# Optimization experiments

Hardware: AMD Instinct MI355X
Metric: run time of the kernel (lower is better)

## Reference

```python
import jax, jax.numpy as jnp
import numpy as np

N = 100000
E = 1600000
IN_DIM = 128
OUT_DIM = 128
NEG_SLOPE = 0.01  # F.leaky_relu default


def setup_inputs() -> dict:
    key = jax.random.key(0)
    k1, k2, k3, k4, k5, k6 = jax.random.split(key, 6)
    feat = jax.random.normal(k1, (N, IN_DIM), dtype=jnp.float32)
    biclique_mask = jax.random.uniform(k2, (IN_DIM,), dtype=jnp.float32)
    W = jax.random.normal(k3, (OUT_DIM, IN_DIM), dtype=jnp.float32) * 0.05
    attn = jax.random.normal(k4, (OUT_DIM,), dtype=jnp.float32) * 0.1
    src = jax.random.randint(k5, (E,), 0, N, dtype=jnp.int32)
    dst = jax.random.randint(k6, (E,), 0, N, dtype=jnp.int32)
    return {"feat": feat, "biclique_mask": biclique_mask, "W": W,
            "attn": attn, "src": src, "dst": dst}


def reference(feat, biclique_mask, W, attn, src, dst):
    # h = Linear(feat * mask), no bias
    h = (feat * biclique_mask[None, :]) @ W.T            # [N, out_dim]
    # edge score depends only on src node -> compute per-node then gather
    s = jax.nn.leaky_relu(h @ attn, negative_slope=NEG_SLOPE)  # [N]
    score = s[src]                                        # [E]
    # edge softmax grouped by destination node
    seg_max = jax.ops.segment_max(score, dst, num_segments=N)  # [N]
    seg_max = jnp.where(jnp.isfinite(seg_max), seg_max, 0.0)   # empty segs
    ex = jnp.exp(score - seg_max[dst])                     # [E]
    denom = jax.ops.segment_sum(ex, dst, num_segments=N)   # [N]
    a = ex / denom[dst]                                    # [E]
    # weighted aggregation: sum_{e: dst(e)=v} h[src(e)] * a[e]
    m = h[src] * a[:, None]                                # [E, out_dim]
    h_new = jax.ops.segment_sum(m, dst, num_segments=N)    # [N, out_dim]
    return jax.nn.relu(h_new)
```

## Files before the change

### kernel.cpp

```cpp
#include <hip/hip_runtime.h>
#include <math.h>

#define NN 100000
#define EE 1600000
#define DIM 128

#define BK 256
#define NBK2 392
#define NCH 256
#define EPB 6250
#define SCN (NBK2 * NCH)
#define NSB 98

#define SRC_MASK 0x1FFFFu

typedef _Float16 half8 __attribute__((ext_vector_type(8)));
typedef float f32x4 __attribute__((ext_vector_type(4)));

__global__ __launch_bounds__(256) void k_wt(const float* __restrict__ W,
                                            const float* __restrict__ mask,
                                            _Float16* __restrict__ Bt) {
    int o = blockIdx.x * 256 + threadIdx.x;
    if (o < DIM * DIM) Bt[o] = (_Float16)(W[o] * mask[o & 127]);
}

__global__ __launch_bounds__(256) void k_gemm(const float* __restrict__ feat,
                                              const _Float16* __restrict__ Bt,
                                              const float* __restrict__ attn,
                                              _Float16* __restrict__ hh,
                                              _Float16* __restrict__ sv16) {
    const int lane = threadIdx.x & 63;
    const int wv   = threadIdx.x >> 6;
    const int l15  = lane & 15;
    const int quad = lane >> 4;
    const int row0 = blockIdx.x * 64 + wv * 16;

    f32x4 acc[8];
#pragma unroll
    for (int nt = 0; nt < 8; ++nt) acc[nt] = (f32x4){0.f, 0.f, 0.f, 0.f};

    const int arow = row0 + l15;
    const bool okA = arow < NN;
    const float* ap = feat + (size_t)(okA ? arow : 0) * DIM + quad * 8;

#pragma unroll
    for (int kc = 0; kc < 4; ++kc) {
        half8 a;
        float4 f0 = ((const float4*)(ap + kc * 32))[0];
        float4 f1 = ((const float4*)(ap + kc * 32))[1];
        if (!okA) { f0 = make_float4(0, 0, 0, 0); f1 = make_float4(0, 0, 0, 0); }
        a[0] = (_Float16)f0.x; a[1] = (_Float16)f0.y;
        a[2] = (_Float16)f0.z; a[3] = (_Float16)f0.w;
        a[4] = (_Float16)f1.x; a[5] = (_Float16)f1.y;
        a[6] = (_Float16)f1.z; a[7] = (_Float16)f1.w;
#pragma unroll
        for (int nt = 0; nt < 8; ++nt) {
            half8 b = *(const half8*)(Bt + (size_t)(nt * 16 + l15) * DIM + kc * 32 + quad * 8);
            acc[nt] = __builtin_amdgcn_mfma_f32_16x16x32_f16(a, b, acc[nt], 0, 0, 0);
        }
    }

    float avv[8];
#pragma unroll
    for (int nt = 0; nt < 8; ++nt) avv[nt] = attn[nt * 16 + l15];

#pragma unroll
    for (int r = 0; r < 4; ++r) {
        int row = row0 + quad * 4 + r;
        float p = 0.f;
#pragma unroll
        for (int nt = 0; nt < 8; ++nt) p += acc[nt][r] * avv[nt];
        p += __shfl_xor(p, 1, 64);
        p += __shfl_xor(p, 2, 64);
        p += __shfl_xor(p, 4, 64);
        p += __shfl_xor(p, 8, 64);
        if (l15 == 0 && row < NN) {
            float lr = (p > 0.f) ? p : 0.01f * p;
            sv16[row] = (_Float16)__expf(lr);
        }
    }

#pragma unroll
    for (int nt = 0; nt < 8; ++nt) {
#pragma unroll
        for (int r = 0; r < 4; ++r) {
            int row = row0 + quad * 4 + r;
            if (row < NN)
                hh[(size_t)row * DIM + nt * 16 + l15] = (_Float16)acc[nt][r];
        }
    }
}

__global__ __launch_bounds__(1024) void k_bhist(const int* __restrict__ dst,
                                                int* __restrict__ gHist) {
    __shared__ int hist[NBK2];
    const int t = threadIdx.x, b = blockIdx.x;
    for (int i = t; i < NBK2; i += 1024) hist[i] = 0;
    __syncthreads();
    const int e0 = b * EPB;
    int e1 = e0 + EPB; if (e1 > EE) e1 = EE;
    for (int e = e0 + t; e < e1; e += 1024)
        atomicAdd(&hist[dst[e] >> 8], 1);
    __syncthreads();
    for (int i = t; i < NBK2; i += 1024)
        gHist[i * NCH + b] = hist[i];
}

__global__ __launch_bounds__(256) void k_scan_a(const int* __restrict__ deg,
                                                int* __restrict__ excl,
                                                int* __restrict__ bsum) {
    __shared__ int wsum[4];
    __shared__ int woff[4];
    const int t = threadIdx.x, b = blockIdx.x;
    const int base = b * 1024 + t * 4;
    int v0 = deg[base + 0];
    int v1 = deg[base + 1];
    int v2 = deg[base + 2];
    int v3 = deg[base + 3];
    int tsum = v0 + v1 + v2 + v3;

    const int lane = t & 63, w = t >> 6;
    int incl = tsum;
#pragma unroll
    for (int d = 1; d < 64; d <<= 1) {
        int n = __shfl_up(incl, d, 64);
        if (lane >= d) incl += n;
    }
    if (lane == 63) wsum[w] = incl;
    __syncthreads();
    if (t == 0) {
        int run = 0;
#pragma unroll
        for (int i = 0; i < 4; ++i) { woff[i] = run; run += wsum[i]; }
        bsum[b] = run;
    }
    __syncthreads();
    int texcl = incl - tsum + woff[w];
    excl[base + 0] = texcl;
    excl[base + 1] = texcl + v0;
    excl[base + 2] = texcl + v0 + v1;
    excl[base + 3] = texcl + v0 + v1 + v2;
}

__global__ __launch_bounds__(128) void k_scan_b(const int* __restrict__ bsum,
                                                int* __restrict__ boff) {
    __shared__ int wtop[2];
    const int t = threadIdx.x;
    const int lane = t & 63, w = t >> 6;
    int v = (t < NSB) ? bsum[t] : 0;
    int incl = v;
#pragma unroll
    for (int d = 1; d < 64; d <<= 1) {
        int n = __shfl_up(incl, d, 64);
        if (lane >= d) incl += n;
    }
    if (lane == 63) wtop[w] = incl;
    __syncthreads();
    int add = (w == 1) ? wtop[0] : 0;
    if (t < NSB) boff[t] = incl - v + add;
}

__global__ __launch_bounds__(1024) void k_bscatter(const int* __restrict__ src,
                                                   const int* __restrict__ dst,
                                                   const int* __restrict__ gOff,
                                                   const int* __restrict__ boff,
                                                   unsigned* __restrict__ binned) {
    __shared__ int cur[NBK2];
    const int t = threadIdx.x, b = blockIdx.x;
    for (int i = t; i < NBK2; i += 1024) {
        int idx = i * NCH + b;
        cur[i] = gOff[idx] + boff[idx >> 10];
    }
    __syncthreads();
    const int e0 = b * EPB;
    int e1 = e0 + EPB; if (e1 > EE) e1 = EE;
    for (int e = e0 + t; e < e1; e += 1024) {
        int d  = dst[e];
        int si = src[e];
        int bk   = d >> 8;
        int dloc = d & (BK - 1);
        int pos = atomicAdd(&cur[bk], 1);
        binned[pos] = (unsigned)si | ((unsigned)dloc << 17);
    }
}

__global__ __launch_bounds__(1024) void k_group(const int* __restrict__ gOff,
                                                const int* __restrict__ boff,
                                                const unsigned* __restrict__ binned,
                                                const _Float16* __restrict__ sv16,
                                                unsigned* __restrict__ pack,
                                                int* __restrict__ offs) {
    __shared__ int ldeg[BK];
    __shared__ int wpart[4];
    const int bk = blockIdx.x;
    const int t  = threadIdx.x;
    const int i0 = bk * NCH;
    const int base = gOff[i0] + boff[i0 >> 10];
    int endp;
    if (bk == NBK2 - 1) endp = EE;
    else {
        int i1 = (bk + 1) * NCH;
        endp = gOff[i1] + boff[i1 >> 10];
    }

    if (t < BK) ldeg[t] = 0;
    __syncthreads();
    for (int j = base + t; j < endp; j += 1024)
        atomicAdd(&ldeg[(binned[j] >> 17) & (BK - 1)], 1);
    __syncthreads();

    int v = 0, incl = 0;
    const int lane = t & 63;
    if (t < BK) {
        v = ldeg[t];
        incl = v;
#pragma unroll
        for (int d = 1; d < 64; d <<= 1) {
            int n = __shfl_up(incl, d, 64);
            if (lane >= d) incl += n;
        }
        if (lane == 63) wpart[t >> 6] = incl;
    }
    __syncthreads();
    if (t == 0) {
        int run = 0;
#pragma unroll
        for (int i = 0; i < 4; ++i) { int tmp = wpart[i]; wpart[i] = run; run += tmp; }
    }
    __syncthreads();
    if (t < BK) {
        int excl = incl - v + wpart[t >> 6];
        int c = base + excl;
        int n = bk * BK + t;
        if (n < NN) offs[n] = c;
        ldeg[t] = c;
    }
    if (bk == NBK2 - 1 && t == 0) offs[NN] = EE;
    __syncthreads();

    for (int j = base + t; j < endp; j += 1024) {
        unsigned e = binned[j];
        int dloc = (e >> 17) & (BK - 1);
        int si   = e & SRC_MASK;
        unsigned short wb =
            __builtin_bit_cast(unsigned short, sv16[si]);
        int pos = atomicAdd(&ldeg[dloc], 1);
        pack[pos] = (unsigned)si | ((unsigned)wb << 17);
    }
}

__global__ __launch_bounds__(256) void k_agg(const _Float16* __restrict__ hh,
                                             const int* __restrict__ offs,
                                             const unsigned* __restrict__ pack,
                                             float* __restrict__ out) {
    const int lane = threadIdx.x & 63;
    const int g    = lane >> 4;
    const int li   = lane & 15;
    const int wid  = __builtin_amdgcn_readfirstlane(blockIdx.x * 4 + (threadIdx.x >> 6));
    if (wid >= NN) return;
    const int beg = __builtin_amdgcn_readfirstlane(offs[wid]);
    const int end = __builtin_amdgcn_readfirstlane(offs[wid + 1]);
    const int deg = end - beg;

    const half8* h8 = (const half8*)hh;
    float acc[8];
#pragma unroll
    for (int k = 0; k < 8; ++k) acc[k] = 0.f;
    float lsum = 0.f;

    for (int base = 0; base < deg; base += 64) {
        const int nrem = deg - base;
        const int idx  = base + lane;
        const int cl   = (idx < deg) ? idx : (deg - 1);
        const unsigned eraw = pack[beg + cl];
        const unsigned enc = (idx < deg) ? eraw : (eraw & SRC_MASK);
        lsum += (float)__builtin_bit_cast(_Float16,
                                          (unsigned short)(enc >> 17));
        const int cmax = (nrem < 64) ? nrem : 64;
        for (int c0 = 0; c0 < cmax; c0 += 16) {
#pragma unroll
            for (int s = 0; s < 4; ++s) {
                const int ei = c0 + s * 4 + g;
                const unsigned eb =
                    (unsigned)__shfl((int)enc, ei, 64);
                const int   si = eb & SRC_MASK;
                const float wg = (float)__builtin_bit_cast(
                    _Float16, (unsigned short)(eb >> 17));
                half8 v = h8[((unsigned)si << 4) + li];
#pragma unroll
                for (int k = 0; k < 8; ++k)
                    acc[k] = fmaf((float)v[k], wg, acc[k]);
            }
        }
    }

#pragma unroll
    for (int k = 0; k < 8; ++k) {
        acc[k] += __shfl_xor(acc[k], 16, 64);
        acc[k] += __shfl_xor(acc[k], 32, 64);
    }
    lsum += __shfl_xor(lsum, 1, 64);
    lsum += __shfl_xor(lsum, 2, 64);
    lsum += __shfl_xor(lsum, 4, 64);
    lsum += __shfl_xor(lsum, 8, 64);
    lsum += __shfl_xor(lsum, 16, 64);
    lsum += __shfl_xor(lsum, 32, 64);

    const float inv = (lsum > 0.f) ? (1.0f / lsum) : 0.f;

    if (g == 0) {
        float4 o0, o1;
        o0.x = fmaxf(acc[0] * inv, 0.f);
        o0.y = fmaxf(acc[1] * inv, 0.f);
        o0.z = fmaxf(acc[2] * inv, 0.f);
        o0.w = fmaxf(acc[3] * inv, 0.f);
        o1.x = fmaxf(acc[4] * inv, 0.f);
        o1.y = fmaxf(acc[5] * inv, 0.f);
        o1.z = fmaxf(acc[6] * inv, 0.f);
        o1.w = fmaxf(acc[7] * inv, 0.f);
        float4* op = (float4*)(out + (size_t)wid * DIM + li * 8);
        op[0] = o0;
        op[1] = o1;
    }
}

extern "C" void kernel_launch(void* const* d_in, const int* in_sizes, int n_in,
                              void* d_out, int out_size, void* d_ws, size_t ws_size,
                              hipStream_t stream) {
    const float* feat = (const float*)d_in[0];
    const float* mask = (const float*)d_in[1];
    const float* W    = (const float*)d_in[2];
    const float* attn = (const float*)d_in[3];
    const int*   src  = (const int*)d_in[4];
    const int*   dst  = (const int*)d_in[5];
    float* out = (float*)d_out;

    char* ws = (char*)d_ws;
    size_t off = 0;
    auto alloc = [&](size_t bytes) -> void* {
        void* p = ws + off;
        off = (off + bytes + 511) & ~(size_t)511;
        return p;
    };
    _Float16* hh   = (_Float16*)alloc((size_t)NN * DIM * 2);
    _Float16* sv16 = (_Float16*)alloc((size_t)NN * 2);
    _Float16* Bt   = (_Float16*)alloc((size_t)DIM * DIM * 2);
    int*     gOff  = (int*)alloc((size_t)SCN * 4);
    int*     offs  = (int*)alloc((size_t)(NN + 1) * 4);
    int*     bsum  = (int*)alloc((size_t)NSB * 4);
    int*     boff  = (int*)alloc((size_t)NSB * 4);
    unsigned* binned = (unsigned*)alloc((size_t)EE * 4);
    unsigned* pack   = (unsigned*)alloc((size_t)EE * 4);

    k_wt<<<(DIM * DIM + 255) / 256, 256, 0, stream>>>(W, mask, Bt);
    k_gemm<<<(NN + 63) / 64, 256, 0, stream>>>(feat, Bt, attn, hh, sv16);
    k_bhist<<<NCH, 1024, 0, stream>>>(dst, gOff);
    k_scan_a<<<NSB, 256, 0, stream>>>(gOff, gOff, bsum);
    k_scan_b<<<1, 128, 0, stream>>>(bsum, boff);
    k_bscatter<<<NCH, 1024, 0, stream>>>(src, dst, gOff, boff, binned);
    k_group<<<NBK2, 1024, 0, stream>>>(gOff, boff, binned, sv16, pack, offs);
    k_agg<<<(NN + 3) / 4, 256, 0, stream>>>(hh, offs, pack, out);
}
```

Measured before the change: 237.6 us.

## Merge GEMM with dst histogram and inline block-offset scan into consumers

The dst-bucket histogram blocks now run as extra blocks of the GEMM launch, so the two independent stages share one grid and can overlap. The tiny single-block scan of block sums is removed, and each bscatter and group block recomputes the 98-entry offset scan in shared memory. This cuts two kernel launches and their serialization gaps. In exchange, every consumer block repeats a small redundant scan and adds extra barriers, and the histogram blocks now use 256 threads instead of 1024.

After: 230.7 us. -2.9%, faster.

```diff
diff --git a/kernel.cpp b/kernel.cpp
--- a/kernel.cpp
+++ b/kernel.cpp
@@ -12,6 +12,8 @@
 #define SCN (NBK2 * NCH)
 #define NSB 98
 
+#define GEMM_BLKS 1563
+
 #define SRC_MASK 0x1FFFFu
 
 typedef _Float16 half8 __attribute__((ext_vector_type(8)));
@@ -24,16 +26,36 @@
     if (o < DIM * DIM) Bt[o] = (_Float16)(W[o] * mask[o & 127]);
 }
 
-__global__ __launch_bounds__(256) void k_gemm(const float* __restrict__ feat,
-                                              const _Float16* __restrict__ Bt,
-                                              const float* __restrict__ attn,
-                                              _Float16* __restrict__ hh,
-                                              _Float16* __restrict__ sv16) {
-    const int lane = threadIdx.x & 63;
-    const int wv   = threadIdx.x >> 6;
+__global__ __launch_bounds__(256) void k_front(const float* __restrict__ feat,
+                                               const _Float16* __restrict__ Bt,
+                                               const float* __restrict__ attn,
+                                               _Float16* __restrict__ hh,
+                                               _Float16* __restrict__ sv16,
+                                               const int* __restrict__ dst,
+                                               int* __restrict__ gHist) {
+    __shared__ int hist[NBK2];
+    const int bx = blockIdx.x;
+    const int t  = threadIdx.x;
+
+    if (bx >= GEMM_BLKS) {
+        const int b = bx - GEMM_BLKS;
+        for (int i = t; i < NBK2; i += 256) hist[i] = 0;
+        __syncthreads();
+        const int e0 = b * EPB;
+        int e1 = e0 + EPB; if (e1 > EE) e1 = EE;
+        for (int e = e0 + t; e < e1; e += 256)
+            atomicAdd(&hist[dst[e] >> 8], 1);
+        __syncthreads();
+        for (int i = t; i < NBK2; i += 256)
+            gHist[i * NCH + b] = hist[i];
+        return;
+    }
+
+    const int lane = t & 63;
+    const int wv   = t >> 6;
     const int l15  = lane & 15;
     const int quad = lane >> 4;
-    const int row0 = blockIdx.x * 64 + wv * 16;
+    const int row0 = bx * 64 + wv * 16;
 
     f32x4 acc[8];
 #pragma unroll
@@ -89,21 +111,6 @@
                 hh[(size_t)row * DIM + nt * 16 + l15] = (_Float16)acc[nt][r];
         }
     }
-}
-
-__global__ __launch_bounds__(1024) void k_bhist(const int* __restrict__ dst,
-                                                int* __restrict__ gHist) {
-    __shared__ int hist[NBK2];
-    const int t = threadIdx.x, b = blockIdx.x;
-    for (int i = t; i < NBK2; i += 1024) hist[i] = 0;
-    __syncthreads();
-    const int e0 = b * EPB;
-    int e1 = e0 + EPB; if (e1 > EE) e1 = EE;
-    for (int e = e0 + t; e < e1; e += 1024)
-        atomicAdd(&hist[dst[e] >> 8], 1);
-    __syncthreads();
-    for (int i = t; i < NBK2; i += 1024)
-        gHist[i * NCH + b] = hist[i];
 }
 
 __global__ __launch_bounds__(256) void k_scan_a(const int* __restrict__ deg,
@@ -142,34 +149,43 @@
     excl[base + 3] = texcl + v0 + v1 + v2;
 }
 
-__global__ __launch_bounds__(128) void k_scan_b(const int* __restrict__ bsum,
-                                                int* __restrict__ boff) {
-    __shared__ int wtop[2];
-    const int t = threadIdx.x;
-    const int lane = t & 63, w = t >> 6;
-    int v = (t < NSB) ? bsum[t] : 0;
-    int incl = v;
-#pragma unroll
-    for (int d = 1; d < 64; d <<= 1) {
-        int n = __shfl_up(incl, d, 64);
-        if (lane >= d) incl += n;
-    }
-    if (lane == 63) wtop[w] = incl;
-    __syncthreads();
-    int add = (w == 1) ? wtop[0] : 0;
-    if (t < NSB) boff[t] = incl - v + add;
-}
+#define INLINE_BOFF_SCAN(bsum, sboff, swtop, t)                          \
+    {                                                                    \
+        const int lane_ = (t) & 63;                                      \
+        int v_ = 0, incl_ = 0;                                           \
+        if ((t) < 128) {                                                 \
+            v_ = ((t) < NSB) ? (bsum)[(t)] : 0;                          \
+            incl_ = v_;                                                  \
+            _Pragma("unroll")                                            \
+            for (int d_ = 1; d_ < 64; d_ <<= 1) {                        \
+                int n_ = __shfl_up(incl_, d_, 64);                       \
+                if (lane_ >= d_) incl_ += n_;                            \
+            }                                                            \
+            if ((t) == 63) (swtop) = incl_;                              \
+        }                                                                \
+        __syncthreads();                                                 \
+        if ((t) < NSB) {                                                 \
+            int add_ = ((t) >= 64) ? (swtop) : 0;                        \
+            (sboff)[(t)] = incl_ - v_ + add_;                            \
+        }                                                                \
+        __syncthreads();                                                 \
+    }
 
 __global__ __launch_bounds__(1024) void k_bscatter(const int* __restrict__ src,
                                                    const int* __restrict__ dst,
                                                    const int* __restrict__ gOff,
-                                                   const int* __restrict__ boff,
+                                                   const int* __restrict__ bsum,
                                                    unsigned* __restrict__ binned) {
     __shared__ int cur[NBK2];
+    __shared__ int sboff[NSB];
+    __shared__ int swtop;
     const int t = threadIdx.x, b = blockIdx.x;
+
+    INLINE_BOFF_SCAN(bsum, sboff, swtop, t)
+
     for (int i = t; i < NBK2; i += 1024) {
         int idx = i * NCH + b;
-        cur[i] = gOff[idx] + boff[idx >> 10];
+        cur[i] = gOff[idx] + sboff[idx >> 10];
     }
     __syncthreads();
     const int e0 = b * EPB;
@@ -185,22 +201,27 @@
 }
 
 __global__ __launch_bounds__(1024) void k_group(const int* __restrict__ gOff,
-                                                const int* __restrict__ boff,
+                                                const int* __restrict__ bsum,
                                                 const unsigned* __restrict__ binned,
                                                 const _Float16* __restrict__ sv16,
                                                 unsigned* __restrict__ pack,
                                                 int* __restrict__ offs) {
     __shared__ int ldeg[BK];
     __shared__ int wpart[4];
+    __shared__ int sboff[NSB];
+    __shared__ int swtop;
     const int bk = blockIdx.x;
     const int t  = threadIdx.x;
+
+    INLINE_BOFF_SCAN(bsum, sboff, swtop, t)
+
     const int i0 = bk * NCH;
-    const int base = gOff[i0] + boff[i0 >> 10];
+    const int base = gOff[i0] + sboff[i0 >> 10];
     int endp;
     if (bk == NBK2 - 1) endp = EE;
     else {
         int i1 = (bk + 1) * NCH;
-        endp = gOff[i1] + boff[i1 >> 10];
+        endp = gOff[i1] + sboff[i1 >> 10];
     }
 
     if (t < BK) ldeg[t] = 0;
@@ -348,16 +369,14 @@
     int*     gOff  = (int*)alloc((size_t)SCN * 4);
     int*     offs  = (int*)alloc((size_t)(NN + 1) * 4);
     int*     bsum  = (int*)alloc((size_t)NSB * 4);
-    int*     boff  = (int*)alloc((size_t)NSB * 4);
     unsigned* binned = (unsigned*)alloc((size_t)EE * 4);
     unsigned* pack   = (unsigned*)alloc((size_t)EE * 4);
 
     k_wt<<<(DIM * DIM + 255) / 256, 256, 0, stream>>>(W, mask, Bt);
-    k_gemm<<<(NN + 63) / 64, 256, 0, stream>>>(feat, Bt, attn, hh, sv16);
-    k_bhist<<<NCH, 1024, 0, stream>>>(dst, gOff);
+    k_front<<<GEMM_BLKS + NCH, 256, 0, stream>>>(feat, Bt, attn, hh, sv16,
+                                                 dst, gOff);
     k_scan_a<<<NSB, 256, 0, stream>>>(gOff, gOff, bsum);
-    k_scan_b<<<1, 128, 0, stream>>>(bsum, boff);
-    k_bscatter<<<NCH, 1024, 0, stream>>>(src, dst, gOff, boff, binned);
-    k_group<<<NBK2, 1024, 0, stream>>>(gOff, boff, binned, sv16, pack, offs);
+    k_bscatter<<<NCH, 1024, 0, stream>>>(src, dst, gOff, bsum, binned);
+    k_group<<<NBK2, 1024, 0, stream>>>(gOff, bsum, binned, sv16, pack, offs);
     k_agg<<<(NN + 3) / 4, 256, 0, stream>>>(hh, offs, pack, out);
 }
```
